# Optimization experiments

Measured on AMD Instinct MI355X. Metric: run time of the kernel, lower is better.

## Reference

```python
import jax, jax.numpy as jnp
import numpy as np

N_USERS = 100000
N_MOVIES = 20000
E = 1000000
D_USER = 128
D_MOVIE = 404
HID = 256
OUT = 128


def setup_inputs() -> dict:
    key = jax.random.key(0)
    ks = jax.random.split(key, 20)
    s = 0.05
    inp = {
        'x_user': jax.random.normal(ks[0], (N_USERS, D_USER), jnp.float32),
        'x_movie': jax.random.normal(ks[1], (N_MOVIES, D_MOVIE), jnp.float32),
        'edge_src': jax.random.randint(ks[2], (E,), 0, N_USERS, jnp.int32),
        'edge_dst': jax.random.randint(ks[3], (E,), 0, N_MOVIES, jnp.int32),
        # layer 1, relation user-rates->movie: lin_l (on aggregated user msgs, with bias), lin_r (root, no bias)
        'w1_rm_l': jax.random.normal(ks[4], (D_USER, HID), jnp.float32) * s,
        'b1_rm': jnp.zeros((HID,), jnp.float32),
        'w1_rm_r': jax.random.normal(ks[5], (D_MOVIE, HID), jnp.float32) * s,
        # layer 1, relation movie-rev_rates->user
        'w1_mu_l': jax.random.normal(ks[6], (D_MOVIE, HID), jnp.float32) * s,
        'b1_mu': jnp.zeros((HID,), jnp.float32),
        'w1_mu_r': jax.random.normal(ks[7], (D_USER, HID), jnp.float32) * s,
        # layer 2, relation user-rates->movie
        'w2_rm_l': jax.random.normal(ks[8], (HID, OUT), jnp.float32) * s,
        'b2_rm': jnp.zeros((OUT,), jnp.float32),
        'w2_rm_r': jax.random.normal(ks[9], (HID, OUT), jnp.float32) * s,
        # layer 2, relation movie-rev_rates->user
        'w2_mu_l': jax.random.normal(ks[10], (HID, OUT), jnp.float32) * s,
        'b2_mu': jnp.zeros((OUT,), jnp.float32),
        'w2_mu_r': jax.random.normal(ks[11], (HID, OUT), jnp.float32) * s,
    }
    return inp


def _seg_mean(msgs, dst, n_dst):
    # mean-aggregate edge messages [E, d] into destination nodes [n_dst, d]
    s = jax.ops.segment_sum(msgs, dst, num_segments=n_dst)
    cnt = jax.ops.segment_sum(jnp.ones((dst.shape[0], 1), msgs.dtype), dst, num_segments=n_dst)
    return s / jnp.maximum(cnt, 1.0)


def _sage(x_src, x_dst, src, dst, n_dst, w_l, b_l, w_r):
    # PyG SAGEConv (mean aggr): lin_l(mean_{j->i} x_j) + lin_r(x_i)
    agg = _seg_mean(x_src[src], dst, n_dst)
    return agg @ w_l + b_l + x_dst @ w_r


def reference(x_user, x_movie, edge_src, edge_dst,
              w1_rm_l, b1_rm, w1_rm_r, w1_mu_l, b1_mu, w1_mu_r,
              w2_rm_l, b2_rm, w2_rm_r, w2_mu_l, b2_mu, w2_mu_r):
    # layer 1 (HeteroConv sum aggr is trivial: one relation per dst type) + relu
    h_movie = jax.nn.relu(_sage(x_user, x_movie, edge_src, edge_dst, N_MOVIES, w1_rm_l, b1_rm, w1_rm_r))
    h_user = jax.nn.relu(_sage(x_movie, x_user, edge_dst, edge_src, N_USERS, w1_mu_l, b1_mu, w1_mu_r))
    # layer 2 (no relu, matching the torch module)
    out_movie = _sage(h_user, h_movie, edge_src, edge_dst, N_MOVIES, w2_rm_l, b2_rm, w2_rm_r)
    out_user = _sage(h_movie, h_user, edge_dst, edge_src, N_USERS, w2_mu_l, b2_mu, w2_mu_r)
    return (out_movie, out_user)
```

## Files before the change

### kernel.cpp

```cpp
#include <hip/hip_runtime.h>
#include <cstddef>
#include <cstdint>

#define E_EDGES 1000000
#define NU 100000
#define NM 20000
#define DU 128
#define DM 404
#define HIDDIM 256
#define OUTDIM 128
#define XMW 544

typedef short bf8_t __attribute__((ext_vector_type(8)));
typedef float f32x4 __attribute__((ext_vector_type(4)));
typedef unsigned short u16x8 __attribute__((ext_vector_type(8)));

__device__ __forceinline__ float b2f(unsigned short u) {
  union { unsigned int i; float f; } x; x.i = ((unsigned int)u) << 16; return x.f;
}
__device__ __forceinline__ unsigned short f2b(float f) {
  union { float f; unsigned int i; } x; x.f = f;
  unsigned int r = x.i + 0x7FFFu + ((x.i >> 16) & 1u);
  return (unsigned short)(r >> 16);
}

#define GLOAD_LDS16(gp, lp)                                                      \
  __builtin_amdgcn_global_load_lds(                                              \
      (const __attribute__((address_space(1))) unsigned int*)(gp),               \
      (__attribute__((address_space(3))) unsigned int*)(lp), 16, 0, 0)

#define HISTB 977
#define PRA 3200000
#define PRB 5280000
#define PRC 5722368
__global__ __launch_bounds__(256) void hist_prep_kernel(
    const int* __restrict__ esrc, const int* __restrict__ edst,
    int* __restrict__ deg_u, int* __restrict__ deg_m,
    int* __restrict__ rank_u, int* __restrict__ rank_m,
    const float* __restrict__ x_user, unsigned short* __restrict__ xu_bf,
    const float* __restrict__ x_movie, unsigned short* __restrict__ xmcat,
    const float* __restrict__ w1_rm_l, const float* __restrict__ w1_rm_r,
    const float* __restrict__ w1_mu_l, const float* __restrict__ w1_mu_r,
    const float* __restrict__ w2_rm_l, const float* __restrict__ w2_mu_r,
    const float* __restrict__ w2_mu_l, const float* __restrict__ w2_rm_r,
    unsigned short* __restrict__ wL1, unsigned short* __restrict__ w1mur,
    unsigned short* __restrict__ wL2u, unsigned short* __restrict__ w2mul,
    unsigned short* __restrict__ w2rmr) {
  if (blockIdx.x < HISTB) {
    int e4 = blockIdx.x * 256 + threadIdx.x;
    if (e4 >= E_EDGES / 4) return;
    int4 s4 = reinterpret_cast<const int4*>(esrc)[e4];
    int4 d4 = reinterpret_cast<const int4*>(edst)[e4];
    int4 ru, rm;
    ru.x = atomicAdd(&deg_u[s4.x], 1);
    ru.y = atomicAdd(&deg_u[s4.y], 1);
    ru.z = atomicAdd(&deg_u[s4.z], 1);
    ru.w = atomicAdd(&deg_u[s4.w], 1);
    rm.x = atomicAdd(&deg_m[d4.x], 1);
    rm.y = atomicAdd(&deg_m[d4.y], 1);
    rm.z = atomicAdd(&deg_m[d4.z], 1);
    rm.w = atomicAdd(&deg_m[d4.w], 1);
    reinterpret_cast<int4*>(rank_u)[e4] = ru;
    reinterpret_cast<int4*>(rank_m)[e4] = rm;
    return;
  }
  int j = (blockIdx.x - HISTB) * 256 + threadIdx.x;
  if (j < PRA) {
    float4 v = reinterpret_cast<const float4*>(x_user)[j];
    ushort4 o;
    o.x = f2b(v.x); o.y = f2b(v.y); o.z = f2b(v.z); o.w = f2b(v.w);
    reinterpret_cast<ushort4*>(xu_bf)[j] = o;
  } else if (j < PRB) {
    int q = j - PRA;
    int row = q / 104, c4 = (q % 104) * 4;
    ushort4 o;
    if (c4 < DM) {
      float4 v = *reinterpret_cast<const float4*>(&x_movie[(size_t)row * DM + c4]);
      o.x = f2b(v.x); o.y = f2b(v.y); o.z = f2b(v.z); o.w = f2b(v.w);
    } else {
      o.x = o.y = o.z = o.w = 0;
    }
    *reinterpret_cast<ushort4*>(&xmcat[(size_t)row * XMW + 128 + c4]) = o;
  } else if (j < PRC) {
    int q = j - PRB;
    if (q < 278528) {
      int n = q / 544, k = q % 544;
      float v = 0.f;
      if (n < 256) {
        if (k < 128) v = w1_rm_l[(size_t)k * 256 + n];
        else if (k < 532) v = w1_rm_r[(size_t)(k - 128) * 256 + n];
      } else {
        if (k >= 128 && k < 532) v = w1_mu_l[(size_t)(k - 128) * 256 + (n - 256)];
      }
      wL1[q] = f2b(v);
    } else if (q < 311296) {
      int p = q - 278528; int n = p / 128, k = p % 128;
      w1mur[p] = f2b(w1_mu_r[(size_t)k * 256 + n]);
    } else if (q < 376832) {
      int p = q - 311296; int n = p / 256, k = p % 256;
      float v = (n < 128) ? w2_rm_l[(size_t)k * 128 + n] : w2_mu_r[(size_t)k * 128 + (n - 128)];
      wL2u[p] = f2b(v);
    } else if (q < 409600) {
      int p = q - 376832; int n = p / 256, k = p % 256;
      w2mul[p] = f2b(w2_mu_l[(size_t)k * 128 + n]);
    } else {
      int p = q - 409600; int n = p / 256, k = p % 256;
      w2rmr[p] = f2b(w2_rm_r[(size_t)k * 128 + n]);
    }
  }
}

__global__ __launch_bounds__(1024) void scan2_kernel(const int* __restrict__ deg_m,
                                                     int* __restrict__ off_m,
                                                     const int* __restrict__ deg_u,
                                                     int* __restrict__ off_u) {
  const int* __restrict__ deg = blockIdx.x ? deg_u : deg_m;
  int* __restrict__ off = blockIdx.x ? off_u : off_m;
  const int n = blockIdx.x ? NU : NM;
  const int tid = threadIdx.x;
  const int lane = tid & 63;
  const int w = tid >> 6;
  __shared__ int wsum[16];
  int carry = 0;
  for (int base = 0; base < n; base += 16384) {
    const int i0 = base + tid * 16;
    int v[16];
    int s = 0;
    if (i0 + 16 <= n) {
#pragma unroll
      for (int q = 0; q < 4; ++q) {
        int4 t4 = *reinterpret_cast<const int4*>(&deg[i0 + q * 4]);
        v[q * 4 + 0] = t4.x; v[q * 4 + 1] = t4.y; v[q * 4 + 2] = t4.z; v[q * 4 + 3] = t4.w;
      }
    } else {
#pragma unroll
      for (int j = 0; j < 16; ++j) v[j] = (i0 + j < n) ? deg[i0 + j] : 0;
    }
#pragma unroll
    for (int j = 0; j < 16; ++j) s += v[j];
    int ws_ = s;
#pragma unroll
    for (int d = 1; d < 64; d <<= 1) {
      int t = __shfl_up(ws_, d, 64);
      if (lane >= d) ws_ += t;
    }
    if (lane == 63) wsum[w] = ws_;
    __syncthreads();
    int woff = 0, ctot = 0;
#pragma unroll
    for (int j = 0; j < 16; ++j) {
      int x = wsum[j];
      if (j < w) woff += x;
      ctot += x;
    }
    int ex = carry + woff + ws_ - s;
    if (i0 + 16 <= n) {
      int o[16];
#pragma unroll
      for (int j = 0; j < 16; ++j) { o[j] = ex; ex += v[j]; }
#pragma unroll
      for (int q = 0; q < 4; ++q)
        *reinterpret_cast<int4*>(&off[i0 + q * 4]) =
            make_int4(o[q * 4], o[q * 4 + 1], o[q * 4 + 2], o[q * 4 + 3]);
    } else {
#pragma unroll
      for (int j = 0; j < 16; ++j) {
        if (i0 + j < n) off[i0 + j] = ex;
        ex += v[j];
      }
    }
    carry += ctot;
    __syncthreads();
  }
  if (tid == 0) off[n] = carry;
}

template <int MODE>
__device__ __forceinline__ void gemm_core(
    const unsigned short* __restrict__ A, int lda,
    const unsigned short* __restrict__ Bt, int ldb, int K,
    const unsigned short* __restrict__ elem, const float* __restrict__ bias,
    void* __restrict__ outA, int M, int bx, int by,
    unsigned short* Alds, unsigned short* Blds) {
  const int tid = threadIdx.x;
  const int w = tid >> 6, l = tid & 63;
  const int row0 = bx * 128;
  const int col0 = by * 128;
  const int wr = w >> 1, wc = w & 1;

  f32x4 acc[4][4] = {};

  int ar0 = row0 + w * 32 + (l >> 2);
  int ar1 = ar0 + 16;
  if (ar0 >= M) ar0 = M - 1;
  if (ar1 >= M) ar1 = M - 1;
  const size_t aoff0 = (size_t)ar0 * lda + (l & 3) * 8;
  const size_t aoff1 = (size_t)ar1 * lda + (l & 3) * 8;
  const int nr0 = col0 + w * 32 + (l >> 2);
  const size_t boff0 = (size_t)nr0 * ldb + (l & 3) * 8;
  const size_t boff1 = (size_t)(nr0 + 16) * ldb + (l & 3) * 8;
  unsigned short* aldsb = &Alds[w * 1024];
  unsigned short* bldsb = &Blds[w * 1024];

  for (int k0 = 0; k0 < K; k0 += 32) {
    GLOAD_LDS16(A + aoff0 + k0, aldsb);
    GLOAD_LDS16(A + aoff1 + k0, aldsb + 512);
    GLOAD_LDS16(Bt + boff0 + k0, bldsb);
    GLOAD_LDS16(Bt + boff1 + k0, bldsb + 512);
    __syncthreads();
    bf8_t af[4], bfr[4];
#pragma unroll
    for (int mi = 0; mi < 4; ++mi)
      af[mi] = *reinterpret_cast<const bf8_t*>(&Alds[(wr * 64 + mi * 16 + (l & 15)) * 32 + (l >> 4) * 8]);
#pragma unroll
    for (int nj = 0; nj < 4; ++nj)
      bfr[nj] = *reinterpret_cast<const bf8_t*>(&Blds[(wc * 64 + nj * 16 + (l & 15)) * 32 + (l >> 4) * 8]);
#pragma unroll
    for (int mi = 0; mi < 4; ++mi)
#pragma unroll
      for (int nj = 0; nj < 4; ++nj)
        acc[mi][nj] = __builtin_amdgcn_mfma_f32_16x16x32_bf16(af[mi], bfr[nj], acc[mi][nj], 0, 0, 0);
    __syncthreads();
  }

#pragma unroll
  for (int mi = 0; mi < 4; ++mi) {
    const int rbase = row0 + wr * 64 + mi * 16 + ((l >> 4) << 2);
#pragma unroll
    for (int nj = 0; nj < 4; ++nj) {
      const int col = col0 + wc * 64 + nj * 16 + (l & 15);
      float bb = 0.0f;
      if constexpr (MODE == 0 || MODE == 1 || MODE == 4) bb = bias[col];
#pragma unroll
      for (int r = 0; r < 4; ++r) {
        const int row = rbase + r;
        if (row >= M) continue;
        float v = acc[mi][nj][r] + bb;
        if constexpr (MODE == 1) v += b2f(elem[(size_t)row * 256 + col]);
        if constexpr (MODE == 4) v += b2f(elem[(size_t)row * 128 + col]);
        if constexpr (MODE == 0 || MODE == 1) v = fmaxf(v, 0.0f);
        if constexpr (MODE == 0 || MODE == 1 || MODE == 5) {
          ((unsigned short*)outA)[(size_t)row * 256 + col] = f2b(v);
        } else if constexpr (MODE == 2) {
          ((unsigned short*)outA)[(size_t)row * 128 + col] = f2b(v);
        } else {
          ((float*)outA)[(size_t)row * 128 + col] = v;
        }
      }
    }
  }
}

#define FILLB 977
__global__ __launch_bounds__(256) void fill_t1_kernel(
    const int* __restrict__ esrc, const int* __restrict__ edst,
    const int* __restrict__ rank_m, const int* __restrict__ rank_u,
    const int* __restrict__ off_m, const int* __restrict__ off_u,
    int* __restrict__ csr_m, int* __restrict__ csr_u,
    const unsigned short* __restrict__ A, const unsigned short* __restrict__ Bt,
    unsigned short* __restrict__ t1) {
  __shared__ unsigned short Alds[128 * 32];
  __shared__ unsigned short Blds[128 * 32];
  if (blockIdx.x < FILLB) {
    int e4 = blockIdx.x * 256 + threadIdx.x;
    if (e4 >= E_EDGES / 4) return;
    int4 s4 = reinterpret_cast<const int4*>(esrc)[e4];
    int4 d4 = reinterpret_cast<const int4*>(edst)[e4];
    int4 rm = reinterpret_cast<const int4*>(rank_m)[e4];
    int4 ru = reinterpret_cast<const int4*>(rank_u)[e4];
    csr_m[off_m[d4.x] + rm.x] = s4.x;
    csr_m[off_m[d4.y] + rm.y] = s4.y;
    csr_m[off_m[d4.z] + rm.z] = s4.z;
    csr_m[off_m[d4.w] + rm.w] = s4.w;
    csr_u[off_u[s4.x] + ru.x] = d4.x;
    csr_u[off_u[s4.y] + ru.y] = d4.y;
    csr_u[off_u[s4.z] + ru.z] = d4.z;
    csr_u[off_u[s4.w] + ru.w] = d4.w;
    return;
  }
  const int bi = blockIdx.x - FILLB;
  gemm_core<5>(A, XMW, Bt, XMW, 416, nullptr, nullptr, t1, NM,
               bi % 157, bi / 157, Alds, Blds);
}

template <int D>
__device__ __forceinline__ void gather_core(
    const unsigned short* __restrict__ table, const int* __restrict__ off,
    const int* __restrict__ idx, unsigned short* __restrict__ out,
    int n, int ostride, int bi) {
  constexpr int LPN = D / 8;
  constexpr int NPB = 256 / LPN;
  const int t = threadIdx.x;
  const int g = t / LPN;
  const int cl = (t % LPN) * 8;
  const int node = bi * NPB + g;
  if (node >= n) return;
  const int beg = off[node], end = off[node + 1];
  const float sc = 1.0f / fmaxf((float)(end - beg), 1.0f);
  float a[8] = {0, 0, 0, 0, 0, 0, 0, 0}, b[8] = {0, 0, 0, 0, 0, 0, 0, 0};
  int p = beg;
  for (; p + 3 < end; p += 4) {
    const int r0 = idx[p], r1 = idx[p + 1], r2 = idx[p + 2], r3 = idx[p + 3];
    u16x8 v0 = *reinterpret_cast<const u16x8*>(&table[(size_t)r0 * D + cl]);
    u16x8 v1 = *reinterpret_cast<const u16x8*>(&table[(size_t)r1 * D + cl]);
    u16x8 v2 = *reinterpret_cast<const u16x8*>(&table[(size_t)r2 * D + cl]);
    u16x8 v3 = *reinterpret_cast<const u16x8*>(&table[(size_t)r3 * D + cl]);
#pragma unroll
    for (int j = 0; j < 8; ++j) { a[j] += b2f(v0[j]); b[j] += b2f(v1[j]); }
#pragma unroll
    for (int j = 0; j < 8; ++j) { a[j] += b2f(v2[j]); b[j] += b2f(v3[j]); }
  }
  for (; p < end; ++p) {
    const int r0 = idx[p];
    u16x8 v0 = *reinterpret_cast<const u16x8*>(&table[(size_t)r0 * D + cl]);
#pragma unroll
    for (int j = 0; j < 8; ++j) a[j] += b2f(v0[j]);
  }
  u16x8 o;
#pragma unroll
  for (int j = 0; j < 8; ++j) o[j] = f2b((a[j] + b[j]) * sc);
  *reinterpret_cast<u16x8*>(&out[(size_t)node * ostride + cl]) = o;
}

__global__ __launch_bounds__(256) void gatherA_kernel(
    const unsigned short* __restrict__ t1, const int* __restrict__ off_u,
    const int* __restrict__ csr_u, unsigned short* __restrict__ M1u,
    const unsigned short* __restrict__ xu, const int* __restrict__ off_m,
    const int* __restrict__ csr_m, unsigned short* __restrict__ xmcat) {
  if (blockIdx.x < 12500)
    gather_core<256>(t1, off_u, csr_u, M1u, NU, 256, blockIdx.x);
  else
    gather_core<128>(xu, off_m, csr_m, xmcat, NM, XMW, blockIdx.x - 12500);
}

__global__ __launch_bounds__(256) void gatherB_kernel(
    const unsigned short* __restrict__ t2, const int* __restrict__ off_u,
    const int* __restrict__ csr_u, unsigned short* __restrict__ M2u,
    const unsigned short* __restrict__ hul, const int* __restrict__ off_m,
    const int* __restrict__ csr_m, unsigned short* __restrict__ M2m) {
  if (blockIdx.x < 6250)
    gather_core<128>(t2, off_u, csr_u, M2u, NU, 128, blockIdx.x);
  else
    gather_core<128>(hul, off_m, csr_m, M2m, NM, 128, blockIdx.x - 6250);
}

__global__ __launch_bounds__(256) void gemmA_kernel(
    const unsigned short* __restrict__ xmcat, const unsigned short* __restrict__ wL1,
    const float* __restrict__ b1_rm, unsigned short* __restrict__ hm,
    const unsigned short* __restrict__ xu, const unsigned short* __restrict__ w1mur,
    const unsigned short* __restrict__ M1u, const float* __restrict__ b1_mu,
    unsigned short* __restrict__ hu) {
  __shared__ unsigned short Alds[128 * 32];
  __shared__ unsigned short Blds[128 * 32];
  if (blockIdx.x < 314) {
    int bi = blockIdx.x;
    gemm_core<0>(xmcat, XMW, wL1, XMW, XMW, nullptr, b1_rm, hm, NM,
                 bi % 157, bi / 157, Alds, Blds);
  } else {
    int bi = blockIdx.x - 314;
    gemm_core<1>(xu, 128, w1mur, 128, 128, M1u, b1_mu, hu, NU,
                 bi % 782, bi / 782, Alds, Blds);
  }
}

__global__ __launch_bounds__(256) void gemmB_kernel(
    const unsigned short* __restrict__ hu, const unsigned short* __restrict__ w2rml,
    unsigned short* __restrict__ hul,
    const unsigned short* __restrict__ hm, const unsigned short* __restrict__ w2mul,
    unsigned short* __restrict__ t2) {
  __shared__ unsigned short Alds[128 * 32];
  __shared__ unsigned short Blds[128 * 32];
  if (blockIdx.x < 782) {
    gemm_core<2>(hu, 256, w2rml, 256, 256, nullptr, nullptr, hul, NU,
                 blockIdx.x, 0, Alds, Blds);
  } else {
    gemm_core<2>(hm, 256, w2mul, 256, 256, nullptr, nullptr, t2, NM,
                 blockIdx.x - 782, 0, Alds, Blds);
  }
}

__global__ __launch_bounds__(256) void gemmC_kernel(
    const unsigned short* __restrict__ hu, const unsigned short* __restrict__ w2mur,
    const unsigned short* __restrict__ M2u, const float* __restrict__ b2_mu,
    float* __restrict__ out_user,
    const unsigned short* __restrict__ hm, const unsigned short* __restrict__ w2rmr,
    const unsigned short* __restrict__ M2m, const float* __restrict__ b2_rm,
    float* __restrict__ out_movie) {
  __shared__ unsigned short Alds[128 * 32];
  __shared__ unsigned short Blds[128 * 32];
  if (blockIdx.x < 782) {
    gemm_core<4>(hu, 256, w2mur, 256, 256, M2u, b2_mu, out_user, NU,
                 blockIdx.x, 0, Alds, Blds);
  } else {
    gemm_core<4>(hm, 256, w2rmr, 256, 256, M2m, b2_rm, out_movie, NM,
                 blockIdx.x - 782, 0, Alds, Blds);
  }
}

extern "C" void kernel_launch(void* const* d_in, const int* in_sizes, int n_in,
                              void* d_out, int out_size, void* d_ws, size_t ws_size,
                              hipStream_t stream) {
  const float* x_user  = (const float*)d_in[0];
  const float* x_movie = (const float*)d_in[1];
  const int*   esrc    = (const int*)d_in[2];
  const int*   edst    = (const int*)d_in[3];
  const float* w1_rm_l = (const float*)d_in[4];
  const float* b1_rm   = (const float*)d_in[5];
  const float* w1_rm_r = (const float*)d_in[6];
  const float* w1_mu_l = (const float*)d_in[7];
  const float* b1_mu   = (const float*)d_in[8];
  const float* w1_mu_r = (const float*)d_in[9];
  const float* w2_rm_l = (const float*)d_in[10];
  const float* b2_rm   = (const float*)d_in[11];
  const float* w2_rm_r = (const float*)d_in[12];
  const float* w2_mu_l = (const float*)d_in[13];
  const float* b2_mu   = (const float*)d_in[14];
  const float* w2_mu_r = (const float*)d_in[15];

  if (ws_size < 214240008ull) return;
  char* wsb = (char*)d_ws;
  unsigned short* xu_bf  = (unsigned short*)(wsb + 0);
  unsigned short* xmcat  = (unsigned short*)(wsb + 25600000);
  unsigned short* hm_bf  = (unsigned short*)(wsb + 47360000);
  unsigned short* t1_bf  = (unsigned short*)(wsb + 57600000);
  unsigned short* M2m_bf = (unsigned short*)(wsb + 57600000);
  unsigned short* t2_bf  = (unsigned short*)(wsb + 67840000);
  unsigned short* M1u_bf = (unsigned short*)(wsb + 72960000);
  unsigned short* hul_bf = (unsigned short*)(wsb + 72960000);
  unsigned short* M2u_bf = (unsigned short*)(wsb + 124160000);
  unsigned short* hu_bf  = (unsigned short*)(wsb + 149760000);
  int* rank_m = (int*)(wsb + 149760000);
  int* rank_u = (int*)(wsb + 153760000);
  unsigned short* wts = (unsigned short*)(wsb + 200960000);
  unsigned short* wL1_t   = wts;
  unsigned short* w1mur_t = wts + 278528;
  unsigned short* wL2u_t  = wts + 311296;
  unsigned short* w2mul_t = wts + 376832;
  unsigned short* w2rmr_t = wts + 409600;
  int* iw    = (int*)(wsb + 201844736);
  int* deg_m = iw;
  int* deg_u = iw + 20000;
  int* off_m = iw + 120000;
  int* off_u = iw + 140004;
  int* csr_m = iw + 240008;
  int* csr_u = iw + 1240008;

  float* out_movie = (float*)d_out;
  float* out_user  = (float*)d_out + (size_t)NM * OUTDIM;

  hipMemsetAsync(deg_m, 0, 120000 * sizeof(int), stream);
  hist_prep_kernel<<<HISTB + (PRC + 255) / 256, 256, 0, stream>>>(
      esrc, edst, deg_u, deg_m, rank_u, rank_m,
      x_user, xu_bf, x_movie, xmcat,
      w1_rm_l, w1_rm_r, w1_mu_l, w1_mu_r, w2_rm_l, w2_mu_r, w2_mu_l, w2_rm_r,
      wL1_t, w1mur_t, wL2u_t, w2mul_t, w2rmr_t);

  scan2_kernel<<<2, 1024, 0, stream>>>(deg_m, off_m, deg_u, off_u);

  fill_t1_kernel<<<FILLB + 314, 256, 0, stream>>>(
      esrc, edst, rank_m, rank_u, off_m, off_u, csr_m, csr_u,
      xmcat + 128, wL1_t + 256 * XMW + 128, t1_bf);

  gatherA_kernel<<<12500 + 1250, 256, 0, stream>>>(
      t1_bf, off_u, csr_u, M1u_bf, xu_bf, off_m, csr_m, xmcat);

  gemmA_kernel<<<314 + 1564, 256, 0, stream>>>(
      xmcat, wL1_t, b1_rm, hm_bf, xu_bf, w1mur_t, M1u_bf, b1_mu, hu_bf);

  gemmB_kernel<<<782 + 157, 256, 0, stream>>>(
      hu_bf, wL2u_t, hul_bf, hm_bf, w2mul_t, t2_bf);

  gatherB_kernel<<<6250 + 1250, 256, 0, stream>>>(
      t2_bf, off_u, csr_u, M2u_bf, hul_bf, off_m, csr_m, M2m_bf);

  gemmC_kernel<<<782 + 157, 256, 0, stream>>>(
      hu_bf, wL2u_t + 128 * 256, M2u_bf, b2_mu, out_user,
      hm_bf, w2rmr_t, M2m_bf, b2_rm, out_movie);
}
```

Before: 475.6 us.

## Merge layer-2 GEMMs and gather directly into fp32 outputs; fold scan into prep

The layer-2 root GEMMs (lin_r plus bias) now run in the same launch as the lin_l GEMMs and write fp32 outputs straight away. The final gather then adds the mean of neighbour messages in place into those outputs, which removes the bf16 M2 intermediates and one kernel launch. The degree histogram is split into its own kernel, and the prefix scan is folded into the prep-conversion kernel as two 256-thread blocks. The trade-offs are that the gather now does a read-modify-write on fp32 outputs, and the scan runs serially in single 256-thread blocks.

```diff
diff --git a/kernel.cpp b/kernel.cpp
--- a/kernel.cpp
+++ b/kernel.cpp
@@ -30,13 +30,93 @@
       (__attribute__((address_space(3))) unsigned int*)(lp), 16, 0, 0)
 
 #define HISTB 977
+__global__ __launch_bounds__(256) void hist_kernel(
+    const int* __restrict__ esrc, const int* __restrict__ edst,
+    int* __restrict__ deg_u, int* __restrict__ deg_m,
+    int* __restrict__ rank_u, int* __restrict__ rank_m) {
+  int e4 = blockIdx.x * 256 + threadIdx.x;
+  if (e4 >= E_EDGES / 4) return;
+  int4 s4 = reinterpret_cast<const int4*>(esrc)[e4];
+  int4 d4 = reinterpret_cast<const int4*>(edst)[e4];
+  int4 ru, rm;
+  ru.x = atomicAdd(&deg_u[s4.x], 1);
+  ru.y = atomicAdd(&deg_u[s4.y], 1);
+  ru.z = atomicAdd(&deg_u[s4.z], 1);
+  ru.w = atomicAdd(&deg_u[s4.w], 1);
+  rm.x = atomicAdd(&deg_m[d4.x], 1);
+  rm.y = atomicAdd(&deg_m[d4.y], 1);
+  rm.z = atomicAdd(&deg_m[d4.z], 1);
+  rm.w = atomicAdd(&deg_m[d4.w], 1);
+  reinterpret_cast<int4*>(rank_u)[e4] = ru;
+  reinterpret_cast<int4*>(rank_m)[e4] = rm;
+}
+
+__device__ __forceinline__ void scan_core_256(const int* __restrict__ deg,
+                                              int* __restrict__ off, int n,
+                                              int* wsum) {
+  const int tid = threadIdx.x;
+  const int lane = tid & 63;
+  const int w = tid >> 6;
+  int carry = 0;
+  for (int base = 0; base < n; base += 4096) {
+    const int i0 = base + tid * 16;
+    int v[16];
+    int s = 0;
+    if (i0 + 16 <= n) {
+#pragma unroll
+      for (int q = 0; q < 4; ++q) {
+        int4 t4 = *reinterpret_cast<const int4*>(&deg[i0 + q * 4]);
+        v[q * 4 + 0] = t4.x; v[q * 4 + 1] = t4.y; v[q * 4 + 2] = t4.z; v[q * 4 + 3] = t4.w;
+      }
+    } else {
+#pragma unroll
+      for (int j = 0; j < 16; ++j) v[j] = (i0 + j < n) ? deg[i0 + j] : 0;
+    }
+#pragma unroll
+    for (int j = 0; j < 16; ++j) s += v[j];
+    int ws_ = s;
+#pragma unroll
+    for (int d = 1; d < 64; d <<= 1) {
+      int t = __shfl_up(ws_, d, 64);
+      if (lane >= d) ws_ += t;
+    }
+    if (lane == 63) wsum[w] = ws_;
+    __syncthreads();
+    int woff = 0, ctot = 0;
+#pragma unroll
+    for (int j = 0; j < 4; ++j) {
+      int x = wsum[j];
+      if (j < w) woff += x;
+      ctot += x;
+    }
+    int ex = carry + woff + ws_ - s;
+    if (i0 + 16 <= n) {
+      int o[16];
+#pragma unroll
+      for (int j = 0; j < 16; ++j) { o[j] = ex; ex += v[j]; }
+#pragma unroll
+      for (int q = 0; q < 4; ++q)
+        *reinterpret_cast<int4*>(&off[i0 + q * 4]) =
+            make_int4(o[q * 4], o[q * 4 + 1], o[q * 4 + 2], o[q * 4 + 3]);
+    } else {
+#pragma unroll
+      for (int j = 0; j < 16; ++j) {
+        if (i0 + j < n) off[i0 + j] = ex;
+        ex += v[j];
+      }
+    }
+    carry += ctot;
+    __syncthreads();
+  }
+  if (tid == 0) off[n] = carry;
+}
+
 #define PRA 3200000
 #define PRB 5280000
 #define PRC 5722368
-__global__ __launch_bounds__(256) void hist_prep_kernel(
-    const int* __restrict__ esrc, const int* __restrict__ edst,
-    int* __restrict__ deg_u, int* __restrict__ deg_m,
-    int* __restrict__ rank_u, int* __restrict__ rank_m,
+__global__ __launch_bounds__(256) void scanprep_kernel(
+    const int* __restrict__ deg_m, int* __restrict__ off_m,
+    const int* __restrict__ deg_u, int* __restrict__ off_u,
     const float* __restrict__ x_user, unsigned short* __restrict__ xu_bf,
     const float* __restrict__ x_movie, unsigned short* __restrict__ xmcat,
     const float* __restrict__ w1_rm_l, const float* __restrict__ w1_rm_r,
@@ -46,25 +126,10 @@
     unsigned short* __restrict__ wL1, unsigned short* __restrict__ w1mur,
     unsigned short* __restrict__ wL2u, unsigned short* __restrict__ w2mul,
     unsigned short* __restrict__ w2rmr) {
-  if (blockIdx.x < HISTB) {
-    int e4 = blockIdx.x * 256 + threadIdx.x;
-    if (e4 >= E_EDGES / 4) return;
-    int4 s4 = reinterpret_cast<const int4*>(esrc)[e4];
-    int4 d4 = reinterpret_cast<const int4*>(edst)[e4];
-    int4 ru, rm;
-    ru.x = atomicAdd(&deg_u[s4.x], 1);
-    ru.y = atomicAdd(&deg_u[s4.y], 1);
-    ru.z = atomicAdd(&deg_u[s4.z], 1);
-    ru.w = atomicAdd(&deg_u[s4.w], 1);
-    rm.x = atomicAdd(&deg_m[d4.x], 1);
-    rm.y = atomicAdd(&deg_m[d4.y], 1);
-    rm.z = atomicAdd(&deg_m[d4.z], 1);
-    rm.w = atomicAdd(&deg_m[d4.w], 1);
-    reinterpret_cast<int4*>(rank_u)[e4] = ru;
-    reinterpret_cast<int4*>(rank_m)[e4] = rm;
-    return;
-  }
-  int j = (blockIdx.x - HISTB) * 256 + threadIdx.x;
+  __shared__ int wsum[4];
+  if (blockIdx.x == 0) { scan_core_256(deg_m, off_m, NM, wsum); return; }
+  if (blockIdx.x == 1) { scan_core_256(deg_u, off_u, NU, wsum); return; }
+  int j = (blockIdx.x - 2) * 256 + threadIdx.x;
   if (j < PRA) {
     float4 v = reinterpret_cast<const float4*>(x_user)[j];
     ushort4 o;
@@ -110,71 +175,6 @@
   }
 }
 
-__global__ __launch_bounds__(1024) void scan2_kernel(const int* __restrict__ deg_m,
-                                                     int* __restrict__ off_m,
-                                                     const int* __restrict__ deg_u,
-                                                     int* __restrict__ off_u) {
-  const int* __restrict__ deg = blockIdx.x ? deg_u : deg_m;
-  int* __restrict__ off = blockIdx.x ? off_u : off_m;
-  const int n = blockIdx.x ? NU : NM;
-  const int tid = threadIdx.x;
-  const int lane = tid & 63;
-  const int w = tid >> 6;
-  __shared__ int wsum[16];
-  int carry = 0;
-  for (int base = 0; base < n; base += 16384) {
-    const int i0 = base + tid * 16;
-    int v[16];
-    int s = 0;
-    if (i0 + 16 <= n) {
-#pragma unroll
-      for (int q = 0; q < 4; ++q) {
-        int4 t4 = *reinterpret_cast<const int4*>(&deg[i0 + q * 4]);
-        v[q * 4 + 0] = t4.x; v[q * 4 + 1] = t4.y; v[q * 4 + 2] = t4.z; v[q * 4 + 3] = t4.w;
-      }
-    } else {
-#pragma unroll
-      for (int j = 0; j < 16; ++j) v[j] = (i0 + j < n) ? deg[i0 + j] : 0;
-    }
-#pragma unroll
-    for (int j = 0; j < 16; ++j) s += v[j];
-    int ws_ = s;
-#pragma unroll
-    for (int d = 1; d < 64; d <<= 1) {
-      int t = __shfl_up(ws_, d, 64);
-      if (lane >= d) ws_ += t;
-    }
-    if (lane == 63) wsum[w] = ws_;
-    __syncthreads();
-    int woff = 0, ctot = 0;
-#pragma unroll
-    for (int j = 0; j < 16; ++j) {
-      int x = wsum[j];
-      if (j < w) woff += x;
-      ctot += x;
-    }
-    int ex = carry + woff + ws_ - s;
-    if (i0 + 16 <= n) {
-      int o[16];
-#pragma unroll
-      for (int j = 0; j < 16; ++j) { o[j] = ex; ex += v[j]; }
-#pragma unroll
-      for (int q = 0; q < 4; ++q)
-        *reinterpret_cast<int4*>(&off[i0 + q * 4]) =
-            make_int4(o[q * 4], o[q * 4 + 1], o[q * 4 + 2], o[q * 4 + 3]);
-    } else {
-#pragma unroll
-      for (int j = 0; j < 16; ++j) {
-        if (i0 + j < n) off[i0 + j] = ex;
-        ex += v[j];
-      }
-    }
-    carry += ctot;
-    __syncthreads();
-  }
-  if (tid == 0) off[n] = carry;
-}
-
 template <int MODE>
 __device__ __forceinline__ void gemm_core(
     const unsigned short* __restrict__ A, int lda,
@@ -230,14 +230,13 @@
     for (int nj = 0; nj < 4; ++nj) {
       const int col = col0 + wc * 64 + nj * 16 + (l & 15);
       float bb = 0.0f;
-      if constexpr (MODE == 0 || MODE == 1 || MODE == 4) bb = bias[col];
+      if constexpr (MODE == 0 || MODE == 1 || MODE == 6) bb = bias[col];
 #pragma unroll
       for (int r = 0; r < 4; ++r) {
         const int row = rbase + r;
         if (row >= M) continue;
         float v = acc[mi][nj][r] + bb;
         if constexpr (MODE == 1) v += b2f(elem[(size_t)row * 256 + col]);
-        if constexpr (MODE == 4) v += b2f(elem[(size_t)row * 128 + col]);
         if constexpr (MODE == 0 || MODE == 1) v = fmaxf(v, 0.0f);
         if constexpr (MODE == 0 || MODE == 1 || MODE == 5) {
           ((unsigned short*)outA)[(size_t)row * 256 + col] = f2b(v);
@@ -322,6 +321,46 @@
   *reinterpret_cast<u16x8*>(&out[(size_t)node * ostride + cl]) = o;
 }
 
+__device__ __forceinline__ void gather_add_f32_128(
+    const unsigned short* __restrict__ table, const int* __restrict__ off,
+    const int* __restrict__ idx, float* __restrict__ out, int n, int bi) {
+  const int t = threadIdx.x;
+  const int g = t >> 4;
+  const int cl = (t & 15) * 8;
+  const int node = bi * 16 + g;
+  if (node >= n) return;
+  const int beg = off[node], end = off[node + 1];
+  const float sc = 1.0f / fmaxf((float)(end - beg), 1.0f);
+  float a[8] = {0, 0, 0, 0, 0, 0, 0, 0}, b[8] = {0, 0, 0, 0, 0, 0, 0, 0};
+  int p = beg;
+  for (; p + 3 < end; p += 4) {
+    const int r0 = idx[p], r1 = idx[p + 1], r2 = idx[p + 2], r3 = idx[p + 3];
+    u16x8 v0 = *reinterpret_cast<const u16x8*>(&table[(size_t)r0 * 128 + cl]);
+    u16x8 v1 = *reinterpret_cast<const u16x8*>(&table[(size_t)r1 * 128 + cl]);
+    u16x8 v2 = *reinterpret_cast<const u16x8*>(&table[(size_t)r2 * 128 + cl]);
+    u16x8 v3 = *reinterpret_cast<const u16x8*>(&table[(size_t)r3 * 128 + cl]);
+#pragma unroll
+    for (int j = 0; j < 8; ++j) { a[j] += b2f(v0[j]); b[j] += b2f(v1[j]); }
+#pragma unroll
+    for (int j = 0; j < 8; ++j) { a[j] += b2f(v2[j]); b[j] += b2f(v3[j]); }
+  }
+  for (; p < end; ++p) {
+    const int r0 = idx[p];
+    u16x8 v0 = *reinterpret_cast<const u16x8*>(&table[(size_t)r0 * 128 + cl]);
+#pragma unroll
+    for (int j = 0; j < 8; ++j) a[j] += b2f(v0[j]);
+  }
+  float* dst = &out[(size_t)node * 128 + cl];
+  float4 o0 = *reinterpret_cast<const float4*>(dst);
+  float4 o1 = *reinterpret_cast<const float4*>(dst + 4);
+  o0.x += (a[0] + b[0]) * sc; o0.y += (a[1] + b[1]) * sc;
+  o0.z += (a[2] + b[2]) * sc; o0.w += (a[3] + b[3]) * sc;
+  o1.x += (a[4] + b[4]) * sc; o1.y += (a[5] + b[5]) * sc;
+  o1.z += (a[6] + b[6]) * sc; o1.w += (a[7] + b[7]) * sc;
+  *reinterpret_cast<float4*>(dst) = o0;
+  *reinterpret_cast<float4*>(dst + 4) = o1;
+}
+
 __global__ __launch_bounds__(256) void gatherA_kernel(
     const unsigned short* __restrict__ t1, const int* __restrict__ off_u,
     const int* __restrict__ csr_u, unsigned short* __restrict__ M1u,
@@ -331,17 +370,6 @@
     gather_core<256>(t1, off_u, csr_u, M1u, NU, 256, blockIdx.x);
   else
     gather_core<128>(xu, off_m, csr_m, xmcat, NM, XMW, blockIdx.x - 12500);
-}
-
-__global__ __launch_bounds__(256) void gatherB_kernel(
-    const unsigned short* __restrict__ t2, const int* __restrict__ off_u,
-    const int* __restrict__ csr_u, unsigned short* __restrict__ M2u,
-    const unsigned short* __restrict__ hul, const int* __restrict__ off_m,
-    const int* __restrict__ csr_m, unsigned short* __restrict__ M2m) {
-  if (blockIdx.x < 6250)
-    gather_core<128>(t2, off_u, csr_u, M2u, NU, 128, blockIdx.x);
-  else
-    gather_core<128>(hul, off_m, csr_m, M2m, NM, 128, blockIdx.x - 6250);
 }
 
 __global__ __launch_bounds__(256) void gemmA_kernel(
@@ -363,38 +391,41 @@
   }
 }
 
-__global__ __launch_bounds__(256) void gemmB_kernel(
+__global__ __launch_bounds__(256) void gemmB2_kernel(
     const unsigned short* __restrict__ hu, const unsigned short* __restrict__ w2rml,
     unsigned short* __restrict__ hul,
     const unsigned short* __restrict__ hm, const unsigned short* __restrict__ w2mul,
-    unsigned short* __restrict__ t2) {
+    unsigned short* __restrict__ t2,
+    const unsigned short* __restrict__ w2mur, const float* __restrict__ b2_mu,
+    float* __restrict__ out_user,
+    const unsigned short* __restrict__ w2rmr, const float* __restrict__ b2_rm,
+    float* __restrict__ out_movie) {
   __shared__ unsigned short Alds[128 * 32];
   __shared__ unsigned short Blds[128 * 32];
   if (blockIdx.x < 782) {
     gemm_core<2>(hu, 256, w2rml, 256, 256, nullptr, nullptr, hul, NU,
                  blockIdx.x, 0, Alds, Blds);
-  } else {
+  } else if (blockIdx.x < 939) {
     gemm_core<2>(hm, 256, w2mul, 256, 256, nullptr, nullptr, t2, NM,
                  blockIdx.x - 782, 0, Alds, Blds);
-  }
-}
-
-__global__ __launch_bounds__(256) void gemmC_kernel(
-    const unsigned short* __restrict__ hu, const unsigned short* __restrict__ w2mur,
-    const unsigned short* __restrict__ M2u, const float* __restrict__ b2_mu,
-    float* __restrict__ out_user,
-    const unsigned short* __restrict__ hm, const unsigned short* __restrict__ w2rmr,
-    const unsigned short* __restrict__ M2m, const float* __restrict__ b2_rm,
-    float* __restrict__ out_movie) {
-  __shared__ unsigned short Alds[128 * 32];
-  __shared__ unsigned short Blds[128 * 32];
-  if (blockIdx.x < 782) {
-    gemm_core<4>(hu, 256, w2mur, 256, 256, M2u, b2_mu, out_user, NU,
-                 blockIdx.x, 0, Alds, Blds);
+  } else if (blockIdx.x < 1721) {
+    gemm_core<6>(hu, 256, w2mur, 256, 256, nullptr, b2_mu, out_user, NU,
+                 blockIdx.x - 939, 0, Alds, Blds);
   } else {
-    gemm_core<4>(hm, 256, w2rmr, 256, 256, M2m, b2_rm, out_movie, NM,
-                 blockIdx.x - 782, 0, Alds, Blds);
-  }
+    gemm_core<6>(hm, 256, w2rmr, 256, 256, nullptr, b2_rm, out_movie, NM,
+                 blockIdx.x - 1721, 0, Alds, Blds);
+  }
+}
+
+__global__ __launch_bounds__(256) void gatherBC_kernel(
+    const unsigned short* __restrict__ t2, const int* __restrict__ off_u,
+    const int* __restrict__ csr_u, float* __restrict__ out_user,
+    const unsigned short* __restrict__ hul, const int* __restrict__ off_m,
+    const int* __restrict__ csr_m, float* __restrict__ out_movie) {
+  if (blockIdx.x < 6250)
+    gather_add_f32_128(t2, off_u, csr_u, out_user, NU, blockIdx.x);
+  else
+    gather_add_f32_128(hul, off_m, csr_m, out_movie, NM, blockIdx.x - 6250);
 }
 
 extern "C" void kernel_launch(void* const* d_in, const int* in_sizes, int n_in,
@@ -423,11 +454,9 @@
   unsigned short* xmcat  = (unsigned short*)(wsb + 25600000);
   unsigned short* hm_bf  = (unsigned short*)(wsb + 47360000);
   unsigned short* t1_bf  = (unsigned short*)(wsb + 57600000);
-  unsigned short* M2m_bf = (unsigned short*)(wsb + 57600000);
   unsigned short* t2_bf  = (unsigned short*)(wsb + 67840000);
   unsigned short* M1u_bf = (unsigned short*)(wsb + 72960000);
   unsigned short* hul_bf = (unsigned short*)(wsb + 72960000);
-  unsigned short* M2u_bf = (unsigned short*)(wsb + 124160000);
   unsigned short* hu_bf  = (unsigned short*)(wsb + 149760000);
   int* rank_m = (int*)(wsb + 149760000);
   int* rank_u = (int*)(wsb + 153760000);
@@ -449,14 +478,14 @@
   float* out_user  = (float*)d_out + (size_t)NM * OUTDIM;
 
   hipMemsetAsync(deg_m, 0, 120000 * sizeof(int), stream);
-  hist_prep_kernel<<<HISTB + (PRC + 255) / 256, 256, 0, stream>>>(
-      esrc, edst, deg_u, deg_m, rank_u, rank_m,
+  hist_kernel<<<HISTB, 256, 0, stream>>>(esrc, edst, deg_u, deg_m, rank_u, rank_m);
+
+  scanprep_kernel<<<2 + (PRC + 255) / 256, 256, 0, stream>>>(
+      deg_m, off_m, deg_u, off_u,
       x_user, xu_bf, x_movie, xmcat,
       w1_rm_l, w1_rm_r, w1_mu_l, w1_mu_r, w2_rm_l, w2_mu_r, w2_mu_l, w2_rm_r,
       wL1_t, w1mur_t, wL2u_t, w2mul_t, w2rmr_t);
 
-  scan2_kernel<<<2, 1024, 0, stream>>>(deg_m, off_m, deg_u, off_u);
-
   fill_t1_kernel<<<FILLB + 314, 256, 0, stream>>>(
       esrc, edst, rank_m, rank_u, off_m, off_u, csr_m, csr_u,
       xmcat + 128, wL1_t + 256 * XMW + 128, t1_bf);
@@ -467,13 +496,10 @@
   gemmA_kernel<<<314 + 1564, 256, 0, stream>>>(
       xmcat, wL1_t, b1_rm, hm_bf, xu_bf, w1mur_t, M1u_bf, b1_mu, hu_bf);
 
-  gemmB_kernel<<<782 + 157, 256, 0, stream>>>(
-      hu_bf, wL2u_t, hul_bf, hm_bf, w2mul_t, t2_bf);
-
-  gatherB_kernel<<<6250 + 1250, 256, 0, stream>>>(
-      t2_bf, off_u, csr_u, M2u_bf, hul_bf, off_m, csr_m, M2m_bf);
-
-  gemmC_kernel<<<782 + 157, 256, 0, stream>>>(
-      hu_bf, wL2u_t + 128 * 256, M2u_bf, b2_mu, out_user,
-      hm_bf, w2rmr_t, M2m_bf, b2_rm, out_movie);
-}
+  gemmB2_kernel<<<1878, 256, 0, stream>>>(
+      hu_bf, wL2u_t, hul_bf, hm_bf, w2mul_t, t2_bf,
+      wL2u_t + 128 * 256, b2_mu, out_user, w2rmr_t, b2_rm, out_movie);
+
+  gatherBC_kernel<<<6250 + 1250, 256, 0, stream>>>(
+      t2_bf, off_u, csr_u, out_user, hul_bf, off_m, csr_m, out_movie);
+}
```

Result: faster. 463.1 us (-2.6%).
